# Kernel optimization log

Hardware: AMD Instinct MI355X
Metric: run time of the kernel (lower is better)

## Reference

```python
import jax, jax.numpy as jnp
import numpy as np

N, E = 50000, 800000
IN_F, OUT_F = 256, 128


def setup_inputs() -> dict:
    key = jax.random.key(0)
    ks = jax.random.split(key, 12)
    s = 1.0 / np.sqrt(OUT_F)
    si = 1.0 / np.sqrt(IN_F)
    return {
        "h": jax.random.normal(ks[0], (N, IN_F), jnp.float32),
        "degrees": jax.random.randint(ks[1], (E, 6), 0, 5).astype(jnp.float32),
        "norm": jax.random.uniform(ks[2], (N, 1), jnp.float32, 0.05, 1.0),
        "src": jax.random.randint(ks[3], (E,), 0, N, jnp.int32),
        "dst": jax.random.randint(ks[4], (E,), 0, N, jnp.int32),
        "W_self": jax.random.normal(ks[5], (IN_F, OUT_F), jnp.float32) * si,
        "b_self": jax.random.normal(ks[6], (OUT_F,), jnp.float32) * si,
        "W_node": jax.random.normal(ks[7], (IN_F, 6 * OUT_F), jnp.float32) * si,
        "b_node": jax.random.normal(ks[8], (6 * OUT_F,), jnp.float32) * si,
        "W_edge": jax.random.normal(ks[9], (6, OUT_F), jnp.float32) * 0.4,
        "bias": jax.random.normal(ks[10], (1, OUT_F), jnp.float32) * 2 * s - s,
    }


def reference(h, degrees, norm, src, dst, W_self, b_self, W_node, b_node, W_edge, bias):
    n = h.shape[0]
    out = W_self.shape[1]
    # node-level linears
    h_node_msg = (h @ W_node + b_node).reshape(n, 6, out)  # [N,6,out]
    h_node_self = h @ W_self + b_self                       # [N,out]
    # edge-level linear (no bias)
    msg = degrees @ W_edge                                  # [E,out]
    mask = (degrees > 0).astype(h.dtype)                    # [E,6]
    # masked sum over the 6 degree-conditioned slices (gather per slice to
    # avoid materializing an [E,6,out] tensor)
    for i in range(6):
        msg = msg + h_node_msg[src, i] * mask[:, i:i + 1]
    msg = msg * norm[src]                                   # src-side norm
    accum = jax.ops.segment_sum(msg, dst, num_segments=n) * norm  # dst-side norm
    return jax.nn.relu(accum + h_node_self + bias)
```

## Files before the change

kernel.cpp:

```cpp
#include <hip/hip_runtime.h>
#include <stdint.h>

#define IN_F 256
#define OUT_F 128
#define NCOLS 1024
#define BM 64
#define BN 128
#define BK 32

using bf16x8 = __attribute__((ext_vector_type(8))) __bf16;
using f32x4  = __attribute__((ext_vector_type(4))) float;

static __device__ __forceinline__ unsigned short f2bf(float f) {
    unsigned u = __float_as_uint(f);
    u = u + 0x7fffu + ((u >> 16) & 1u);
    return (unsigned short)(u >> 16);
}
static __device__ __forceinline__ float bf_lo(unsigned u) { return __uint_as_float(u << 16); }
static __device__ __forceinline__ float bf_hi(unsigned u) { return __uint_as_float(u & 0xffff0000u); }

static __device__ __forceinline__ void async_load16(const void* g, void* l) {
    __builtin_amdgcn_global_load_lds(
        (__attribute__((address_space(1))) void*)g,
        (__attribute__((address_space(3))) void*)l,
        16, 0, 0);
}

__global__ void k_conv_h(const float* __restrict__ h, unsigned short* __restrict__ hb, int total8) {
    int i = blockIdx.x * blockDim.x + threadIdx.x;
    if (i >= total8) return;
    const float4* src = ((const float4*)h) + (size_t)i * 2;
    float4 a = src[0], b = src[1];
    union { unsigned short us[8]; uint4 v; } u;
    u.us[0] = f2bf(a.x); u.us[1] = f2bf(a.y); u.us[2] = f2bf(a.z); u.us[3] = f2bf(a.w);
    u.us[4] = f2bf(b.x); u.us[5] = f2bf(b.y); u.us[6] = f2bf(b.z); u.us[7] = f2bf(b.w);
    ((uint4*)hb)[i] = u.v;
}

__global__ void k_conv_w(const float* __restrict__ Wn, const float* __restrict__ Ws,
                         unsigned short* __restrict__ Wt, int total) {
    int i = blockIdx.x * blockDim.x + threadIdx.x;
    if (i >= total) return;
    int k = i >> 10, c = i & 1023;
    float v;
    if (c < 768) {
        v = Wn[(size_t)k * 768 + c];
    } else if (c < 896) {
        int j = c - 768; v = 0.f;
#pragma unroll
        for (int s = 0; s < 6; ++s) v += Wn[(size_t)k * 768 + s * 128 + j];
    } else {
        v = Ws[(size_t)k * 128 + (c - 896)];
    }
    Wt[(size_t)c * IN_F + k] = f2bf(v);
}

__global__ void k_conv_b(const float* __restrict__ bn, const float* __restrict__ bs,
                         float* __restrict__ bvec) {
    int c = blockIdx.x * blockDim.x + threadIdx.x;
    if (c >= NCOLS) return;
    float v;
    if (c < 768) v = bn[c];
    else if (c < 896) {
        int j = c - 768; v = 0.f;
#pragma unroll
        for (int s = 0; s < 6; ++s) v += bn[s * 128 + j];
    } else v = bs[c - 896];
    bvec[c] = v;
}

__global__ void __launch_bounds__(256) k_gemm(
    const unsigned short* __restrict__ hb,
    const unsigned short* __restrict__ Wt,
    const float* __restrict__ bvec,
    const float* __restrict__ norm,
    unsigned short* __restrict__ P, int N, int rowsPerXcd)
{
    __shared__ char lds[(BM + BN) * BK * 2];
    __shared__ unsigned short Pst[BM * BN];
    char* Ab = lds;
    char* Bb = lds + BM * BK * 2;

    const int f  = blockIdx.x;
    const int xc = f & 7;
    const int j  = f >> 3;
    const int rs = xc * rowsPerXcd + (j >> 3);
    const int ct = j & 7;
    const int r0 = rs * BM;
    if (r0 >= N) return;
    const int c0 = ct * BN;

    const int tid = threadIdx.x;
    const int wid = tid >> 6, lane = tid & 63;
    const int lrow = lane & 15, s = lane >> 4;
    const int wr = wid >> 1, wc = wid & 1;

    const int arow = tid >> 2;
    const int achunk = (tid & 3) ^ ((arow >> 1) & 3);
    int agrow = r0 + arow; if (agrow >= N) agrow = N - 1;
    const unsigned short* aseg = hb + (size_t)agrow * IN_F + achunk * 8;

    const int bcol0 = tid >> 2;
    const int bchunk0 = (tid & 3) ^ ((bcol0 >> 1) & 3);
    const unsigned short* bseg0 = Wt + (size_t)(c0 + bcol0) * IN_F + bchunk0 * 8;
    const int idx1 = tid + 256;
    const int bcol1 = idx1 >> 2;
    const int bchunk1 = (idx1 & 3) ^ ((bcol1 >> 1) & 3);
    const unsigned short* bseg1 = Wt + (size_t)(c0 + bcol1) * IN_F + bchunk1 * 8;

    int a_off[2], b_off[4];
#pragma unroll
    for (int m = 0; m < 2; ++m) {
        int rl = wr * 32 + m * 16 + lrow;
        a_off[m] = rl * 64 + ((s ^ ((rl >> 1) & 3)) << 4);
    }
#pragma unroll
    for (int n = 0; n < 4; ++n) {
        int cl = wc * 64 + n * 16 + lrow;
        b_off[n] = cl * 64 + ((s ^ ((cl >> 1) & 3)) << 4);
    }

    float nrmv[2][4];
#pragma unroll
    for (int m = 0; m < 2; ++m)
#pragma unroll
        for (int r = 0; r < 4; ++r) {
            int rg = r0 + wr * 32 + m * 16 + s * 4 + r;
            nrmv[m][r] = norm[rg < N ? rg : N - 1];
        }

    f32x4 acc[2][4] = {};

    for (int kk = 0; kk < IN_F / BK; ++kk) {
        async_load16(aseg + kk * BK, Ab + tid * 16);
        async_load16(bseg0 + kk * BK, Bb + tid * 16);
        async_load16(bseg1 + kk * BK, Bb + (tid + 256) * 16);
        __syncthreads();

        bf16x8 af[2], bfv[4];
#pragma unroll
        for (int m = 0; m < 2; ++m) af[m] = *(const bf16x8*)(Ab + a_off[m]);
#pragma unroll
        for (int n = 0; n < 4; ++n) bfv[n] = *(const bf16x8*)(Bb + b_off[n]);
#pragma unroll
        for (int m = 0; m < 2; ++m)
#pragma unroll
            for (int n = 0; n < 4; ++n)
                acc[m][n] = __builtin_amdgcn_mfma_f32_16x16x32_bf16(af[m], bfv[n], acc[m][n], 0, 0, 0);
        __syncthreads();
    }

    const bool doNorm = (c0 < 896);
#pragma unroll
    for (int m = 0; m < 2; ++m) {
        const int rowl = wr * 32 + m * 16 + s * 4;
#pragma unroll
        for (int n = 0; n < 4; ++n) {
            const int col = wc * 64 + n * 16 + lrow;
            const float bv = bvec[c0 + col];
            const int chunk = col >> 3, cb = col & 7;
#pragma unroll
            for (int r = 0; r < 4; ++r) {
                float v = acc[m][n][r] + bv;
                if (doNorm) v *= nrmv[m][r];
                const int row = rowl + r;
                Pst[row * 128 + ((chunk ^ (row & 7)) * 8 + cb)] = f2bf(v);
            }
        }
    }
    __syncthreads();

    const int ch = tid & 15;
#pragma unroll
    for (int rr = 0; rr < 4; ++rr) {
        const int rl = rr * 16 + (tid >> 4);
        const int rg = r0 + rl;
        if (rg < N) {
            uint4 v = *(const uint4*)&Pst[rl * 128 + ((ch ^ (rl & 7)) * 8)];
            *(uint4*)(P + (size_t)rg * NCOLS + c0 + ch * 8) = v;
        }
    }
}

__global__ void k_hist(const int* __restrict__ dst, int* __restrict__ counts, int E) {
    int e = blockIdx.x * blockDim.x + threadIdx.x;
    if (e < E) atomicAdd(&counts[dst[e]], 1);
}

__global__ void __launch_bounds__(256) k_scan_a(const int* __restrict__ counts,
                                                int* __restrict__ offs,
                                                int* __restrict__ bsum, int N) {
    __shared__ int sm[256];
    int tid = threadIdx.x;
    int i = blockIdx.x * 256 + tid;
    int v = (i < N) ? counts[i] : 0;
    sm[tid] = v;
    __syncthreads();
#pragma unroll
    for (int st = 1; st < 256; st <<= 1) {
        int t = (tid >= st) ? sm[tid - st] : 0;
        __syncthreads();
        sm[tid] += t;
        __syncthreads();
    }
    if (i < N) offs[i] = sm[tid] - v;
    if (tid == 255) bsum[blockIdx.x] = sm[255];
}

__global__ void __launch_bounds__(256) k_scan_b(int* __restrict__ bsum, int NB) {
    __shared__ int sm[256];
    int tid = threadIdx.x;
    int v = (tid < NB) ? bsum[tid] : 0;
    sm[tid] = v;
    __syncthreads();
#pragma unroll
    for (int st = 1; st < 256; st <<= 1) {
        int t = (tid >= st) ? sm[tid - st] : 0;
        __syncthreads();
        sm[tid] += t;
        __syncthreads();
    }
    if (tid < NB) bsum[tid] = sm[tid] - v;
}

__global__ void k_scan_c(int* __restrict__ offs, const int* __restrict__ bsum,
                         int* __restrict__ cursor, int N) {
    int i = blockIdx.x * 256 + threadIdx.x;
    if (i >= N) return;
    int o = offs[i] + bsum[blockIdx.x];
    offs[i] = o;
    cursor[i] = o;
}

__global__ void k_scatter(const int* __restrict__ src, const int* __restrict__ dst,
                          const float* __restrict__ degrees,
                          int* __restrict__ cursor, uint2* __restrict__ pedge, int E) {
    int e = blockIdx.x * blockDim.x + threadIdx.x;
    if (e >= E) return;
    int d = dst[e];
    int slot = atomicAdd(&cursor[d], 1);
    unsigned pk = 0;
#pragma unroll
    for (int i = 0; i < 6; ++i) {
        float df = degrees[(size_t)e * 6 + i];
        pk |= ((unsigned)df) << (4 * i);
    }
    pedge[slot] = make_uint2((unsigned)src[e], pk);
}

__global__ void __launch_bounds__(256) k_aggregate(
    const unsigned short* __restrict__ P,
    const int* __restrict__ row_start, const int* __restrict__ counts,
    const uint2* __restrict__ pedge,
    const float* __restrict__ norm, const float* __restrict__ W_edge,
    const float* __restrict__ bias, float* __restrict__ out, int N)
{
    __shared__ unsigned EL[4][192];
    const int wid = threadIdx.x >> 6;
    const int n = blockIdx.x * 4 + wid;
    if (n >= N) return;
    const int lane = threadIdx.x & 63;
    unsigned* el = EL[wid];

    float2 w[6];
#pragma unroll
    for (int i = 0; i < 6; ++i) w[i] = *(const float2*)(W_edge + i * OUT_F + lane * 2);

    const int beg = row_start[n];
    const int end = beg + counts[n];
    const unsigned* __restrict__ Pd = (const unsigned*)P;

    float Swd[6] = {0.f, 0.f, 0.f, 0.f, 0.f, 0.f};
    float g0 = 0.f, g1 = 0.f;

    for (int p0 = beg; p0 < end; p0 += 64) {
        const int t = p0 + lane;
        const bool valid = t < end;
        uint2 pe = valid ? pedge[t] : make_uint2(0u, 0u);
        const unsigned dp = pe.y;
        const float nr = (dp != 0u) ? norm[pe.x] : 0.f;

        unsigned zm = 0;
#pragma unroll
        for (int i = 0; i < 6; ++i) {
            int d = (dp >> (4 * i)) & 15;
            if (d == 0) zm |= (1u << i);
            Swd[i] += nr * (float)d;
        }
        const int z = __popc(zm);
        const int ne = (dp == 0u) ? 0 : ((z <= 2) ? (1 + z) : (6 - z));

        int x = ne;
#pragma unroll
        for (int st = 1; st < 64; st <<= 1) {
            int v = __shfl_up(x, st);
            if (lane >= st) x += v;
        }
        const int excl = x - ne;
        const int total = __shfl(x, 63);

        if (ne) {
            const unsigned base = pe.x * 512u;
            int wp = excl;
            if (z <= 2) {
                el[wp++] = base + 384u;
#pragma unroll
                for (int i = 0; i < 6; ++i)
                    if ((zm >> i) & 1u) el[wp++] = (base + i * 64u) | 0x80000000u;
            } else {
#pragma unroll
                for (int i = 0; i < 6; ++i)
                    if (!((zm >> i) & 1u)) el[wp++] = base + i * 64u;
            }
        }
        asm volatile("s_waitcnt lgkmcnt(0)" ::: "memory");

        int j = 0;
        for (; j + 4 <= total; j += 4) {
            unsigned e0 = el[j], e1 = el[j + 1], e2 = el[j + 2], e3 = el[j + 3];
            unsigned u0 = Pd[(e0 & 0x7fffffffu) + lane];
            unsigned u1 = Pd[(e1 & 0x7fffffffu) + lane];
            unsigned u2 = Pd[(e2 & 0x7fffffffu) + lane];
            unsigned u3 = Pd[(e3 & 0x7fffffffu) + lane];
            float s0 = __uint_as_float(0x3f800000u | (e0 & 0x80000000u));
            float s1 = __uint_as_float(0x3f800000u | (e1 & 0x80000000u));
            float s2 = __uint_as_float(0x3f800000u | (e2 & 0x80000000u));
            float s3 = __uint_as_float(0x3f800000u | (e3 & 0x80000000u));
            g0 += s0 * bf_lo(u0); g1 += s0 * bf_hi(u0);
            g0 += s1 * bf_lo(u1); g1 += s1 * bf_hi(u1);
            g0 += s2 * bf_lo(u2); g1 += s2 * bf_hi(u2);
            g0 += s3 * bf_lo(u3); g1 += s3 * bf_hi(u3);
        }
        for (; j < total; ++j) {
            unsigned e0 = el[j];
            unsigned u0 = Pd[(e0 & 0x7fffffffu) + lane];
            float s0 = __uint_as_float(0x3f800000u | (e0 & 0x80000000u));
            g0 += s0 * bf_lo(u0); g1 += s0 * bf_hi(u0);
        }
    }

    float b0 = 0.f, b1 = 0.f;
#pragma unroll
    for (int i = 0; i < 6; ++i) {
        float v = Swd[i];
#pragma unroll
        for (int st = 1; st < 64; st <<= 1) v += __shfl_xor(v, st);
        b0 += v * w[i].x;
        b1 += v * w[i].y;
    }

    const unsigned us = Pd[(size_t)n * 512 + 448 + lane];
    const float nd = norm[n];
    const float2 bv = *(const float2*)(bias + lane * 2);
    float2 o;
    o.x = fmaxf((g0 + b0) * nd + bf_lo(us) + bv.x, 0.f);
    o.y = fmaxf((g1 + b1) * nd + bf_hi(us) + bv.y, 0.f);
    *(float2*)(out + (size_t)n * OUT_F + lane * 2) = o;
}

extern "C" void kernel_launch(void* const* d_in, const int* in_sizes, int n_in,
                              void* d_out, int out_size, void* d_ws, size_t ws_size,
                              hipStream_t stream)
{
    const float* h       = (const float*)d_in[0];
    const float* degrees = (const float*)d_in[1];
    const float* norm    = (const float*)d_in[2];
    const int*   src     = (const int*)d_in[3];
    const int*   dst     = (const int*)d_in[4];
    const float* W_self  = (const float*)d_in[5];
    const float* b_self  = (const float*)d_in[6];
    const float* W_node  = (const float*)d_in[7];
    const float* b_node  = (const float*)d_in[8];
    const float* W_edge  = (const float*)d_in[9];
    const float* bias    = (const float*)d_in[10];
    float* out = (float*)d_out;

    const int N = in_sizes[2];
    const int E = in_sizes[3];
    const int NB = (N + 255) / 256;

    char* ws = (char*)d_ws;
    size_t off = 0;
    auto alloc = [&](size_t sz) { size_t o = off; off = (off + sz + 255) & ~(size_t)255; return o; };
    unsigned short* P      = (unsigned short*)(ws + alloc((size_t)N * NCOLS * 2));
    unsigned short* hb     = (unsigned short*)(ws + alloc((size_t)N * IN_F * 2));
    unsigned short* Wt     = (unsigned short*)(ws + alloc((size_t)NCOLS * IN_F * 2));
    float*          bvec   = (float*)(ws + alloc(NCOLS * 4));
    int*            counts = (int*)(ws + alloc((size_t)N * 4));
    int*            offs   = (int*)(ws + alloc((size_t)N * 4));
    int*            cursor = (int*)(ws + alloc((size_t)N * 4));
    int*            bsum   = (int*)(ws + alloc((size_t)NB * 4));
    uint2*          pedge  = (uint2*)(ws + alloc((size_t)E * 8));

    hipMemsetAsync(counts, 0, (size_t)N * 4, stream);

    int t8 = N * (IN_F / 8);
    k_conv_h<<<(t8 + 255) / 256, 256, 0, stream>>>(h, hb, t8);

    int tw = IN_F * NCOLS;
    k_conv_w<<<(tw + 255) / 256, 256, 0, stream>>>(W_node, W_self, Wt, tw);
    k_conv_b<<<(NCOLS + 255) / 256, 256, 0, stream>>>(b_node, b_self, bvec);

    const int R  = (N + BM - 1) / BM;
    const int RP = (R + 7) / 8;
    k_gemm<<<RP * 8 * 8, 256, 0, stream>>>(hb, Wt, bvec, norm, P, N, RP);

    k_hist<<<(E + 255) / 256, 256, 0, stream>>>(dst, counts, E);
    k_scan_a<<<NB, 256, 0, stream>>>(counts, offs, bsum, N);
    k_scan_b<<<1, 256, 0, stream>>>(bsum, NB);
    k_scan_c<<<NB, 256, 0, stream>>>(offs, bsum, cursor, N);
    k_scatter<<<(E + 255) / 256, 256, 0, stream>>>(src, dst, degrees, cursor, pedge, E);

    k_aggregate<<<(N + 3) / 4, 256, 0, stream>>>(P, offs, counts, pedge, norm, W_edge, bias, out, N);
}
```

Before: 233.3 us.

## Store per-slice node messages in FP8 and split gather lists by precision

The six per-slice projected node messages are now written as FP8 (e4m3) instead of bf16. The summed-slice and self columns stay bf16 in a 1280-byte row layout. The aggregate kernel keeps separate edge lists for the bf16 sum entries and the FP8 slice entries, so the slice gathers move half the bytes. The GEMM epilogue writes directly to global memory without LDS staging, and the bias-conversion kernel is folded into the weight-conversion kernel. FP8 storage lowers message precision and risks accuracy-tolerance failures. The direct, less coalesced stores may also cost some GEMM write efficiency.

After: 248.8 us. 1.07x slower.

```diff
diff --git a/kernel.cpp b/kernel.cpp
--- a/kernel.cpp
+++ b/kernel.cpp
@@ -4,12 +4,14 @@
 #define IN_F 256
 #define OUT_F 128
 #define NCOLS 1024
+#define PROW 1280
 #define BM 64
 #define BN 128
 #define BK 32
 
 using bf16x8 = __attribute__((ext_vector_type(8))) __bf16;
 using f32x4  = __attribute__((ext_vector_type(4))) float;
+using f32x2  = __attribute__((ext_vector_type(2))) float;
 
 static __device__ __forceinline__ unsigned short f2bf(float f) {
     unsigned u = __float_as_uint(f);
@@ -38,7 +40,8 @@
 }
 
 __global__ void k_conv_w(const float* __restrict__ Wn, const float* __restrict__ Ws,
-                         unsigned short* __restrict__ Wt, int total) {
+                         const float* __restrict__ bn, const float* __restrict__ bs,
+                         unsigned short* __restrict__ Wt, float* __restrict__ bvec, int total) {
     int i = blockIdx.x * blockDim.x + threadIdx.x;
     if (i >= total) return;
     int k = i >> 10, c = i & 1023;
@@ -53,20 +56,17 @@
         v = Ws[(size_t)k * 128 + (c - 896)];
     }
     Wt[(size_t)c * IN_F + k] = f2bf(v);
-}
-
-__global__ void k_conv_b(const float* __restrict__ bn, const float* __restrict__ bs,
-                         float* __restrict__ bvec) {
-    int c = blockIdx.x * blockDim.x + threadIdx.x;
-    if (c >= NCOLS) return;
-    float v;
-    if (c < 768) v = bn[c];
-    else if (c < 896) {
-        int j = c - 768; v = 0.f;
-#pragma unroll
-        for (int s = 0; s < 6; ++s) v += bn[s * 128 + j];
-    } else v = bs[c - 896];
-    bvec[c] = v;
+
+    if (i < NCOLS) {
+        float b;
+        if (i < 768) b = bn[i];
+        else if (i < 896) {
+            int j = i - 768; b = 0.f;
+#pragma unroll
+            for (int s = 0; s < 6; ++s) b += bn[s * 128 + j];
+        } else b = bs[i - 896];
+        bvec[i] = b;
+    }
 }
 
 __global__ void __launch_bounds__(256) k_gemm(
@@ -74,10 +74,9 @@
     const unsigned short* __restrict__ Wt,
     const float* __restrict__ bvec,
     const float* __restrict__ norm,
-    unsigned short* __restrict__ P, int N, int rowsPerXcd)
+    char* __restrict__ PG, int N, int rowsPerXcd)
 {
     __shared__ char lds[(BM + BN) * BK * 2];
-    __shared__ unsigned short Pst[BM * BN];
     char* Ab = lds;
     char* Bb = lds + BM * BK * 2;
 
@@ -150,34 +149,46 @@
         __syncthreads();
     }
 
-    const bool doNorm = (c0 < 896);
-#pragma unroll
-    for (int m = 0; m < 2; ++m) {
-        const int rowl = wr * 32 + m * 16 + s * 4;
-#pragma unroll
-        for (int n = 0; n < 4; ++n) {
-            const int col = wc * 64 + n * 16 + lrow;
-            const float bv = bvec[c0 + col];
-            const int chunk = col >> 3, cb = col & 7;
+    float bvn[4];
+#pragma unroll
+    for (int n = 0; n < 4; ++n) bvn[n] = bvec[c0 + wc * 64 + n * 16 + lrow];
+
+    if (ct < 6) {
+#pragma unroll
+        for (int m = 0; m < 2; ++m) {
 #pragma unroll
             for (int r = 0; r < 4; ++r) {
-                float v = acc[m][n][r] + bv;
-                if (doNorm) v *= nrmv[m][r];
-                const int row = rowl + r;
-                Pst[row * 128 + ((chunk ^ (row & 7)) * 8 + cb)] = f2bf(v);
+                const int rg = r0 + wr * 32 + m * 16 + s * 4 + r;
+                const float sc = nrmv[m][r];
+                float v0 = (acc[m][0][r] + bvn[0]) * sc;
+                float v1 = (acc[m][1][r] + bvn[1]) * sc;
+                float v2 = (acc[m][2][r] + bvn[2]) * sc;
+                float v3 = (acc[m][3][r] + bvn[3]) * sc;
+                int d = __builtin_amdgcn_cvt_pk_fp8_f32(v0, v1, 0, false);
+                d = __builtin_amdgcn_cvt_pk_fp8_f32(v2, v3, d, true);
+                if (rg < N)
+                    *(int*)(PG + (size_t)rg * PROW + ct * 128 + (wc * 16 + lrow) * 4) = d;
             }
         }
-    }
-    __syncthreads();
-
-    const int ch = tid & 15;
-#pragma unroll
-    for (int rr = 0; rr < 4; ++rr) {
-        const int rl = rr * 16 + (tid >> 4);
-        const int rg = r0 + rl;
-        if (rg < N) {
-            uint4 v = *(const uint4*)&Pst[rl * 128 + ((ch ^ (rl & 7)) * 8)];
-            *(uint4*)(P + (size_t)rg * NCOLS + c0 + ch * 8) = v;
+    } else {
+        const bool doN = (ct == 6);
+        const int boff = doN ? 768 : 1024;
+#pragma unroll
+        for (int m = 0; m < 2; ++m) {
+#pragma unroll
+            for (int r = 0; r < 4; ++r) {
+                const int rg = r0 + wr * 32 + m * 16 + s * 4 + r;
+                const float sc = doN ? nrmv[m][r] : 1.f;
+                float v0 = (acc[m][0][r] + bvn[0]) * sc;
+                float v1 = (acc[m][1][r] + bvn[1]) * sc;
+                float v2 = (acc[m][2][r] + bvn[2]) * sc;
+                float v3 = (acc[m][3][r] + bvn[3]) * sc;
+                uint2 dd;
+                dd.x = (unsigned)f2bf(v0) | ((unsigned)f2bf(v1) << 16);
+                dd.y = (unsigned)f2bf(v2) | ((unsigned)f2bf(v3) << 16);
+                if (rg < N)
+                    *(uint2*)(PG + (size_t)rg * PROW + boff + (wc * 32 + 2 * lrow) * 4) = dd;
+            }
         }
     }
 }
@@ -249,34 +260,40 @@
 }
 
 __global__ void __launch_bounds__(256) k_aggregate(
-    const unsigned short* __restrict__ P,
+    const char* __restrict__ PG,
     const int* __restrict__ row_start, const int* __restrict__ counts,
     const uint2* __restrict__ pedge,
     const float* __restrict__ norm, const float* __restrict__ W_edge,
     const float* __restrict__ bias, float* __restrict__ out, int N)
 {
-    __shared__ unsigned EL[4][192];
+    __shared__ unsigned ELS[4][64];
+    __shared__ unsigned ELF[4][192];
     const int wid = threadIdx.x >> 6;
     const int n = blockIdx.x * 4 + wid;
     if (n >= N) return;
     const int lane = threadIdx.x & 63;
-    unsigned* el = EL[wid];
-
-    float2 w[6];
-#pragma unroll
-    for (int i = 0; i < 6; ++i) w[i] = *(const float2*)(W_edge + i * OUT_F + lane * 2);
+    unsigned* els = ELS[wid];
+    unsigned* elf = ELF[wid];
+
+    const int cA = (lane >> 5) * 64 + (lane & 1) * 32 + ((lane >> 1) & 15);
+    const int cB = cA + 16;
+
+    float wA[6], wB[6];
+#pragma unroll
+    for (int i = 0; i < 6; ++i) {
+        wA[i] = W_edge[i * OUT_F + cA];
+        wB[i] = W_edge[i * OUT_F + cB];
+    }
 
     const int beg = row_start[n];
     const int end = beg + counts[n];
-    const unsigned* __restrict__ Pd = (const unsigned*)P;
 
     float Swd[6] = {0.f, 0.f, 0.f, 0.f, 0.f, 0.f};
     float g0 = 0.f, g1 = 0.f;
 
     for (int p0 = beg; p0 < end; p0 += 64) {
         const int t = p0 + lane;
-        const bool valid = t < end;
-        uint2 pe = valid ? pedge[t] : make_uint2(0u, 0u);
+        uint2 pe = (t < end) ? pedge[t] : make_uint2(0u, 0u);
         const unsigned dp = pe.y;
         const float nr = (dp != 0u) ? norm[pe.x] : 0.f;
 
@@ -288,54 +305,82 @@
             Swd[i] += nr * (float)d;
         }
         const int z = __popc(zm);
-        const int ne = (dp == 0u) ? 0 : ((z <= 2) ? (1 + z) : (6 - z));
-
-        int x = ne;
+        int ns, nf;
+        if (dp == 0u)      { ns = 0; nf = 0; }
+        else if (z <= 2)   { ns = 1; nf = z; }
+        else               { ns = 0; nf = 6 - z; }
+
+        int x = (ns << 16) | nf;
 #pragma unroll
         for (int st = 1; st < 64; st <<= 1) {
             int v = __shfl_up(x, st);
             if (lane >= st) x += v;
         }
-        const int excl = x - ne;
-        const int total = __shfl(x, 63);
-
-        if (ne) {
-            const unsigned base = pe.x * 512u;
-            int wp = excl;
+        const int tot = __shfl(x, 63);
+        x -= (ns << 16) | nf;
+        const int exS = x >> 16, exF = x & 0xffff;
+        const int totS = tot >> 16, totF = tot & 0xffff;
+
+        if (dp != 0u) {
+            const unsigned base = pe.x * (unsigned)PROW;
             if (z <= 2) {
-                el[wp++] = base + 384u;
+                els[exS] = base + 768u;
+                int wp = exF;
 #pragma unroll
                 for (int i = 0; i < 6; ++i)
-                    if ((zm >> i) & 1u) el[wp++] = (base + i * 64u) | 0x80000000u;
+                    if ((zm >> i) & 1u) elf[wp++] = (base + i * 128u) | 0x80000000u;
             } else {
+                int wp = exF;
 #pragma unroll
                 for (int i = 0; i < 6; ++i)
-                    if (!((zm >> i) & 1u)) el[wp++] = base + i * 64u;
+                    if (!((zm >> i) & 1u)) elf[wp++] = base + i * 128u;
             }
         }
         asm volatile("s_waitcnt lgkmcnt(0)" ::: "memory");
 
         int j = 0;
-        for (; j + 4 <= total; j += 4) {
-            unsigned e0 = el[j], e1 = el[j + 1], e2 = el[j + 2], e3 = el[j + 3];
-            unsigned u0 = Pd[(e0 & 0x7fffffffu) + lane];
-            unsigned u1 = Pd[(e1 & 0x7fffffffu) + lane];
-            unsigned u2 = Pd[(e2 & 0x7fffffffu) + lane];
-            unsigned u3 = Pd[(e3 & 0x7fffffffu) + lane];
+        for (; j + 4 <= totS; j += 4) {
+            unsigned a0 = els[j], a1 = els[j + 1], a2 = els[j + 2], a3 = els[j + 3];
+            unsigned u0 = *(const unsigned*)(PG + a0 + lane * 4);
+            unsigned u1 = *(const unsigned*)(PG + a1 + lane * 4);
+            unsigned u2 = *(const unsigned*)(PG + a2 + lane * 4);
+            unsigned u3 = *(const unsigned*)(PG + a3 + lane * 4);
+            g0 += bf_lo(u0); g1 += bf_hi(u0);
+            g0 += bf_lo(u1); g1 += bf_hi(u1);
+            g0 += bf_lo(u2); g1 += bf_hi(u2);
+            g0 += bf_lo(u3); g1 += bf_hi(u3);
+        }
+        for (; j < totS; ++j) {
+            unsigned u0 = *(const unsigned*)(PG + els[j] + lane * 4);
+            g0 += bf_lo(u0); g1 += bf_hi(u0);
+        }
+
+        j = 0;
+        for (; j + 4 <= totF; j += 4) {
+            unsigned e0 = elf[j], e1 = elf[j + 1], e2 = elf[j + 2], e3 = elf[j + 3];
+            unsigned short q0 = *(const unsigned short*)(PG + (e0 & 0x7fffffffu) + lane * 2);
+            unsigned short q1 = *(const unsigned short*)(PG + (e1 & 0x7fffffffu) + lane * 2);
+            unsigned short q2 = *(const unsigned short*)(PG + (e2 & 0x7fffffffu) + lane * 2);
+            unsigned short q3 = *(const unsigned short*)(PG + (e3 & 0x7fffffffu) + lane * 2);
+            f32x2 f0 = __builtin_amdgcn_cvt_pk_f32_fp8((int)q0, false);
+            f32x2 f1 = __builtin_amdgcn_cvt_pk_f32_fp8((int)q1, false);
+            f32x2 f2 = __builtin_amdgcn_cvt_pk_f32_fp8((int)q2, false);
+            f32x2 f3 = __builtin_amdgcn_cvt_pk_f32_fp8((int)q3, false);
             float s0 = __uint_as_float(0x3f800000u | (e0 & 0x80000000u));
             float s1 = __uint_as_float(0x3f800000u | (e1 & 0x80000000u));
             float s2 = __uint_as_float(0x3f800000u | (e2 & 0x80000000u));
             float s3 = __uint_as_float(0x3f800000u | (e3 & 0x80000000u));
-            g0 += s0 * bf_lo(u0); g1 += s0 * bf_hi(u0);
-            g0 += s1 * bf_lo(u1); g1 += s1 * bf_hi(u1);
-            g0 += s2 * bf_lo(u2); g1 += s2 * bf_hi(u2);
-            g0 += s3 * bf_lo(u3); g1 += s3 * bf_hi(u3);
-        }
-        for (; j < total; ++j) {
-            unsigned e0 = el[j];
-            unsigned u0 = Pd[(e0 & 0x7fffffffu) + lane];
+            g0 += s0 * f0.x; g1 += s0 * f0.y;
+            g0 += s1 * f1.x; g1 += s1 * f1.y;
+            g0 += s2 * f2.x; g1 += s2 * f2.y;
+            g0 += s3 * f3.x; g1 += s3 * f3.y;
+        }
+        for (; j < totF; ++j) {
+            unsigned e0 = elf[j];
+            unsigned short q0 = *(const unsigned short*)(PG + (e0 & 0x7fffffffu) + lane * 2);
+            f32x2 f0 = __builtin_amdgcn_cvt_pk_f32_fp8((int)q0, false);
             float s0 = __uint_as_float(0x3f800000u | (e0 & 0x80000000u));
-            g0 += s0 * bf_lo(u0); g1 += s0 * bf_hi(u0);
+            g0 += s0 * f0.x; g1 += s0 * f0.y;
         }
     }
 
@@ -345,17 +390,16 @@
         float v = Swd[i];
 #pragma unroll
         for (int st = 1; st < 64; st <<= 1) v += __shfl_xor(v, st);
-        b0 += v * w[i].x;
-        b1 += v * w[i].y;
-    }
-
-    const unsigned us = Pd[(size_t)n * 512 + 448 + lane];
+        b0 += v * wA[i];
+        b1 += v * wB[i];
+    }
+
+    const unsigned us = *(const unsigned*)(PG + (size_t)n * PROW + 1024 + lane * 4);
     const float nd = norm[n];
-    const float2 bv = *(const float2*)(bias + lane * 2);
-    float2 o;
-    o.x = fmaxf((g0 + b0) * nd + bf_lo(us) + bv.x, 0.f);
-    o.y = fmaxf((g1 + b1) * nd + bf_hi(us) + bv.y, 0.f);
-    *(float2*)(out + (size_t)n * OUT_F + lane * 2) = o;
+    float o0 = fmaxf((g0 + b0) * nd + bf_lo(us) + bias[cA], 0.f);
+    float o1 = fmaxf((g1 + b1) * nd + bf_hi(us) + bias[cB], 0.f);
+    out[(size_t)n * OUT_F + cA] = o0;
+    out[(size_t)n * OUT_F + cB] = o1;
 }
 
 extern "C" void kernel_launch(void* const* d_in, const int* in_sizes, int n_in,
@@ -382,7 +426,7 @@
     char* ws = (char*)d_ws;
     size_t off = 0;
     auto alloc = [&](size_t sz) { size_t o = off; off = (off + sz + 255) & ~(size_t)255; return o; };
-    unsigned short* P      = (unsigned short*)(ws + alloc((size_t)N * NCOLS * 2));
+    char*           PG     = (char*)(ws + alloc((size_t)N * PROW));
     unsigned short* hb     = (unsigned short*)(ws + alloc((size_t)N * IN_F * 2));
     unsigned short* Wt     = (unsigned short*)(ws + alloc((size_t)NCOLS * IN_F * 2));
     float*          bvec   = (float*)(ws + alloc(NCOLS * 4));
@@ -398,12 +442,11 @@
     k_conv_h<<<(t8 + 255) / 256, 256, 0, stream>>>(h, hb, t8);
 
     int tw = IN_F * NCOLS;
-    k_conv_w<<<(tw + 255) / 256, 256, 0, stream>>>(W_node, W_self, Wt, tw);
-    k_conv_b<<<(NCOLS + 255) / 256, 256, 0, stream>>>(b_node, b_self, bvec);
+    k_conv_w<<<(tw + 255) / 256, 256, 0, stream>>>(W_node, W_self, b_node, b_self, Wt, bvec, tw);
 
     const int R  = (N + BM - 1) / BM;
     const int RP = (R + 7) / 8;
-    k_gemm<<<RP * 8 * 8, 256, 0, stream>>>(hb, Wt, bvec, norm, P, N, RP);
+    k_gemm<<<RP * 8 * 8, 256, 0, stream>>>(hb, Wt, bvec, norm, PG, N, RP);
 
     k_hist<<<(E + 255) / 256, 256, 0, stream>>>(dst, counts, E);
     k_scan_a<<<NB, 256, 0, stream>>>(counts, offs, bsum, N);
@@ -411,5 +454,5 @@
     k_scan_c<<<NB, 256, 0, stream>>>(offs, bsum, cursor, N);
     k_scatter<<<(E + 255) / 256, 256, 0, stream>>>(src, dst, degrees, cursor, pedge, E);
 
-    k_aggregate<<<(N + 3) / 4, 256, 0, stream>>>(P, offs, counts, pedge, norm, W_edge, bias, out, N);
-}
+    k_aggregate<<<(N + 3) / 4, 256, 0, stream>>>(PG, offs, counts, pedge, norm, W_edge, bias, out, N);
+}
```

## Precompute per-edge gather entries and degree sums during scatter

Applied to the files above, without the earlier changes.

Moves the expansion of each edge into row-offset gather entries out of the aggregate kernel and into the CSR scatter kernel, so the histogram counts entries rather than edges. The norm-weighted degree sums per destination are accumulated with float atomics into a new N×6 buffer, which removes the per-node wave reductions in aggregate. The aggregate loop now just stages entries into LDS and gathers, and the bias conversion kernel is folded into the weight conversion. In exchange there are many more atomics in scatter, an extra memset, and nondeterministic float summation order.

Result: slower. 413.3 us (+77.1%).

```diff
diff --git a/kernel.cpp b/kernel.cpp
--- a/kernel.cpp
+++ b/kernel.cpp
@@ -24,6 +24,14 @@
         (__attribute__((address_space(1))) void*)g,
         (__attribute__((address_space(3))) void*)l,
         16, 0, 0);
+}
+
+static __device__ __forceinline__ int edge_ne(const float* dg, unsigned& zm) {
+    zm = 0;
+#pragma unroll
+    for (int i = 0; i < 6; ++i) if (!(dg[i] > 0.f)) zm |= (1u << i);
+    int z = __popc(zm);
+    return (z == 6) ? 0 : ((z <= 2) ? (1 + z) : (6 - z));
 }
 
 __global__ void k_conv_h(const float* __restrict__ h, unsigned short* __restrict__ hb, int total8) {
@@ -38,7 +46,8 @@
 }
 
 __global__ void k_conv_w(const float* __restrict__ Wn, const float* __restrict__ Ws,
-                         unsigned short* __restrict__ Wt, int total) {
+                         const float* __restrict__ bn, const float* __restrict__ bs,
+                         unsigned short* __restrict__ Wt, float* __restrict__ bvec, int total) {
     int i = blockIdx.x * blockDim.x + threadIdx.x;
     if (i >= total) return;
     int k = i >> 10, c = i & 1023;
@@ -53,20 +62,17 @@
         v = Ws[(size_t)k * 128 + (c - 896)];
     }
     Wt[(size_t)c * IN_F + k] = f2bf(v);
-}
-
-__global__ void k_conv_b(const float* __restrict__ bn, const float* __restrict__ bs,
-                         float* __restrict__ bvec) {
-    int c = blockIdx.x * blockDim.x + threadIdx.x;
-    if (c >= NCOLS) return;
-    float v;
-    if (c < 768) v = bn[c];
-    else if (c < 896) {
-        int j = c - 768; v = 0.f;
-#pragma unroll
-        for (int s = 0; s < 6; ++s) v += bn[s * 128 + j];
-    } else v = bs[c - 896];
-    bvec[c] = v;
+
+    if (i < NCOLS) {
+        float b;
+        if (i < 768) b = bn[i];
+        else if (i < 896) {
+            int j = i - 768; b = 0.f;
+#pragma unroll
+            for (int s = 0; s < 6; ++s) b += bn[s * 128 + j];
+        } else b = bs[i - 896];
+        bvec[i] = b;
+    }
 }
 
 __global__ void __launch_bounds__(256) k_gemm(
@@ -182,9 +188,16 @@
     }
 }
 
-__global__ void k_hist(const int* __restrict__ dst, int* __restrict__ counts, int E) {
+__global__ void k_hist(const int* __restrict__ dst, const float* __restrict__ degrees,
+                       int* __restrict__ counts, int E) {
     int e = blockIdx.x * blockDim.x + threadIdx.x;
-    if (e < E) atomicAdd(&counts[dst[e]], 1);
+    if (e >= E) return;
+    float dg[6];
+#pragma unroll
+    for (int i = 0; i < 6; ++i) dg[i] = degrees[(size_t)e * 6 + i];
+    unsigned zm;
+    int ne = edge_ne(dg, zm);
+    if (ne) atomicAdd(&counts[dst[e]], ne);
 }
 
 __global__ void __launch_bounds__(256) k_scan_a(const int* __restrict__ counts,
@@ -233,120 +246,92 @@
 }
 
 __global__ void k_scatter(const int* __restrict__ src, const int* __restrict__ dst,
-                          const float* __restrict__ degrees,
-                          int* __restrict__ cursor, uint2* __restrict__ pedge, int E) {
+                          const float* __restrict__ degrees, const float* __restrict__ norm,
+                          float* __restrict__ D, int* __restrict__ cursor,
+                          unsigned* __restrict__ entries, int E) {
     int e = blockIdx.x * blockDim.x + threadIdx.x;
     if (e >= E) return;
-    int d = dst[e];
-    int slot = atomicAdd(&cursor[d], 1);
-    unsigned pk = 0;
-#pragma unroll
-    for (int i = 0; i < 6; ++i) {
-        float df = degrees[(size_t)e * 6 + i];
-        pk |= ((unsigned)df) << (4 * i);
-    }
-    pedge[slot] = make_uint2((unsigned)src[e], pk);
+    const int d = dst[e];
+    const int s = src[e];
+    float dg[6];
+#pragma unroll
+    for (int i = 0; i < 6; ++i) dg[i] = degrees[(size_t)e * 6 + i];
+    unsigned zm;
+    const int ne = edge_ne(dg, zm);
+    const int z = __popc(zm);
+    const float nr = norm[s];
+
+#pragma unroll
+    for (int i = 0; i < 6; ++i)
+        if (dg[i] > 0.f) atomicAdd(&D[(size_t)d * 6 + i], nr * dg[i]);
+
+    if (ne == 0) return;
+    int slot = atomicAdd(&cursor[d], ne);
+    const unsigned base = (unsigned)s * 512u;
+    if (z <= 2) {
+        entries[slot++] = base + 384u;
+#pragma unroll
+        for (int i = 0; i < 6; ++i)
+            if ((zm >> i) & 1u) entries[slot++] = (base + i * 64u) | 0x80000000u;
+    } else {
+#pragma unroll
+        for (int i = 0; i < 6; ++i)
+            if (!((zm >> i) & 1u)) entries[slot++] = base + i * 64u;
+    }
 }
 
 __global__ void __launch_bounds__(256) k_aggregate(
-    const unsigned short* __restrict__ P,
+    const unsigned* __restrict__ Pd,
     const int* __restrict__ row_start, const int* __restrict__ counts,
-    const uint2* __restrict__ pedge,
+    const unsigned* __restrict__ entries,
+    const float* __restrict__ D,
     const float* __restrict__ norm, const float* __restrict__ W_edge,
     const float* __restrict__ bias, float* __restrict__ out, int N)
 {
-    __shared__ unsigned EL[4][192];
+    __shared__ unsigned EB[4][64];
     const int wid = threadIdx.x >> 6;
     const int n = blockIdx.x * 4 + wid;
     if (n >= N) return;
     const int lane = threadIdx.x & 63;
-    unsigned* el = EL[wid];
-
-    float2 w[6];
-#pragma unroll
-    for (int i = 0; i < 6; ++i) w[i] = *(const float2*)(W_edge + i * OUT_F + lane * 2);
+    unsigned* eb = EB[wid];
+
+    float b0 = 0.f, b1 = 0.f;
+#pragma unroll
+    for (int i = 0; i < 6; ++i) {
+        const float dv = D[(size_t)n * 6 + i];
+        float2 w = *(const float2*)(W_edge + i * OUT_F + lane * 2);
+        b0 = fmaf(dv, w.x, b0);
+        b1 = fmaf(dv, w.y, b1);
+    }
 
     const int beg = row_start[n];
     const int end = beg + counts[n];
-    const unsigned* __restrict__ Pd = (const unsigned*)P;
-
-    float Swd[6] = {0.f, 0.f, 0.f, 0.f, 0.f, 0.f};
     float g0 = 0.f, g1 = 0.f;
 
     for (int p0 = beg; p0 < end; p0 += 64) {
-        const int t = p0 + lane;
-        const bool valid = t < end;
-        uint2 pe = valid ? pedge[t] : make_uint2(0u, 0u);
-        const unsigned dp = pe.y;
-        const float nr = (dp != 0u) ? norm[pe.x] : 0.f;
-
-        unsigned zm = 0;
-#pragma unroll
-        for (int i = 0; i < 6; ++i) {
-            int d = (dp >> (4 * i)) & 15;
-            if (d == 0) zm |= (1u << i);
-            Swd[i] += nr * (float)d;
-        }
-        const int z = __popc(zm);
-        const int ne = (dp == 0u) ? 0 : ((z <= 2) ? (1 + z) : (6 - z));
-
-        int x = ne;
-#pragma unroll
-        for (int st = 1; st < 64; st <<= 1) {
-            int v = __shfl_up(x, st);
-            if (lane >= st) x += v;
-        }
-        const int excl = x - ne;
-        const int total = __shfl(x, 63);
-
-        if (ne) {
-            const unsigned base = pe.x * 512u;
-            int wp = excl;
-            if (z <= 2) {
-                el[wp++] = base + 384u;
-#pragma unroll
-                for (int i = 0; i < 6; ++i)
-                    if ((zm >> i) & 1u) el[wp++] = (base + i * 64u) | 0x80000000u;
-            } else {
-#pragma unroll
-                for (int i = 0; i < 6; ++i)
-                    if (!((zm >> i) & 1u)) el[wp++] = base + i * 64u;
+        if (p0 + lane < end) eb[lane] = entries[p0 + lane];
+        asm volatile("s_waitcnt lgkmcnt(0)" ::: "memory");
+        __builtin_amdgcn_sched_barrier(0);
+
+        const int cnt = min(64, end - p0);
+        int j = 0;
+        for (; j + 8 <= cnt; j += 8) {
+#pragma unroll
+            for (int q = 0; q < 8; ++q) {
+                unsigned e0 = eb[j + q];
+                unsigned u0 = Pd[(e0 & 0x7fffffffu) + lane];
+                float s0 = __uint_as_float(0x3f800000u | (e0 & 0x80000000u));
+                g0 = fmaf(s0, bf_lo(u0), g0);
+                g1 = fmaf(s0, bf_hi(u0), g1);
             }
         }
-        asm volatile("s_waitcnt lgkmcnt(0)" ::: "memory");
-
-        int j = 0;
-        for (; j + 4 <= total; j += 4) {
-            unsigned e0 = el[j], e1 = el[j + 1], e2 = el[j + 2], e3 = el[j + 3];
-            unsigned u0 = Pd[(e0 & 0x7fffffffu) + lane];
-            unsigned u1 = Pd[(e1 & 0x7fffffffu) + lane];
-            unsigned u2 = Pd[(e2 & 0x7fffffffu) + lane];
-            unsigned u3 = Pd[(e3 & 0x7fffffffu) + lane];
-            float s0 = __uint_as_float(0x3f800000u | (e0 & 0x80000000u));
-            float s1 = __uint_as_float(0x3f800000u | (e1 & 0x80000000u));
-            float s2 = __uint_as_float(0x3f800000u | (e2 & 0x80000000u));
-            float s3 = __uint_as_float(0x3f800000u | (e3 & 0x80000000u));
-            g0 += s0 * bf_lo(u0); g1 += s0 * bf_hi(u0);
-            g0 += s1 * bf_lo(u1); g1 += s1 * bf_hi(u1);
-            g0 += s2 * bf_lo(u2); g1 += s2 * bf_hi(u2);
-            g0 += s3 * bf_lo(u3); g1 += s3 * bf_hi(u3);
-        }
-        for (; j < total; ++j) {
-            unsigned e0 = el[j];
+        for (; j < cnt; ++j) {
+            unsigned e0 = eb[j];
             unsigned u0 = Pd[(e0 & 0x7fffffffu) + lane];
             float s0 = __uint_as_float(0x3f800000u | (e0 & 0x80000000u));
-            g0 += s0 * bf_lo(u0); g1 += s0 * bf_hi(u0);
+            g0 = fmaf(s0, bf_lo(u0), g0);
+            g1 = fmaf(s0, bf_hi(u0), g1);
         }
-    }
-
-    float b0 = 0.f, b1 = 0.f;
-#pragma unroll
-    for (int i = 0; i < 6; ++i) {
-        float v = Swd[i];
-#pragma unroll
-        for (int st = 1; st < 64; st <<= 1) v += __shfl_xor(v, st);
-        b0 += v * w[i].x;
-        b1 += v * w[i].y;
     }
 
     const unsigned us = Pd[(size_t)n * 512 + 448 + lane];
@@ -386,30 +371,32 @@
     unsigned short* hb     = (unsigned short*)(ws + alloc((size_t)N * IN_F * 2));
     unsigned short* Wt     = (unsigned short*)(ws + alloc((size_t)NCOLS * IN_F * 2));
     float*          bvec   = (float*)(ws + alloc(NCOLS * 4));
+    float*          D      = (float*)(ws + alloc((size_t)N * 6 * 4));
     int*            counts = (int*)(ws + alloc((size_t)N * 4));
     int*            offs   = (int*)(ws + alloc((size_t)N * 4));
     int*            cursor = (int*)(ws + alloc((size_t)N * 4));
     int*            bsum   = (int*)(ws + alloc((size_t)NB * 4));
-    uint2*          pedge  = (uint2*)(ws + alloc((size_t)E * 8));
+    unsigned*       entries= (unsigned*)(ws + alloc((size_t)E * 3 * 4));
 
     hipMemsetAsync(counts, 0, (size_t)N * 4, stream);
+    hipMemsetAsync(D, 0, (size_t)N * 6 * 4, stream);
 
     int t8 = N * (IN_F / 8);
     k_conv_h<<<(t8 + 255) / 256, 256, 0, stream>>>(h, hb, t8);
 
     int tw = IN_F * NCOLS;
-    k_conv_w<<<(tw + 255) / 256, 256, 0, stream>>>(W_node, W_self, Wt, tw);
-    k_conv_b<<<(NCOLS + 255) / 256, 256, 0, stream>>>(b_node, b_self, bvec);
+    k_conv_w<<<(tw + 255) / 256, 256, 0, stream>>>(W_node, W_self, b_node, b_self, Wt, bvec, tw);
 
     const int R  = (N + BM - 1) / BM;
     const int RP = (R + 7) / 8;
     k_gemm<<<RP * 8 * 8, 256, 0, stream>>>(hb, Wt, bvec, norm, P, N, RP);
 
-    k_hist<<<(E + 255) / 256, 256, 0, stream>>>(dst, counts, E);
+    k_hist<<<(E + 255) / 256, 256, 0, stream>>>(dst, degrees, counts, E);
     k_scan_a<<<NB, 256, 0, stream>>>(counts, offs, bsum, N);
     k_scan_b<<<1, 256, 0, stream>>>(bsum, NB);
     k_scan_c<<<NB, 256, 0, stream>>>(offs, bsum, cursor, N);
-    k_scatter<<<(E + 255) / 256, 256, 0, stream>>>(src, dst, degrees, cursor, pedge, E);
-
-    k_aggregate<<<(N + 3) / 4, 256, 0, stream>>>(P, offs, counts, pedge, norm, W_edge, bias, out, N);
-}
+    k_scatter<<<(E + 255) / 256, 256, 0, stream>>>(src, dst, degrees, norm, D, cursor, entries, E);
+
+    k_aggregate<<<(N + 3) / 4, 256, 0, stream>>>((const unsigned*)P, offs, counts, entries, D,
+                                                 norm, W_edge, bias, out, N);
+}
```
